# Kernel tuning notes

Measured on AMD Instinct MI355X. Metric: run time of the kernel, lower is better.

The kernel has to match this reference:

```python
import jax, jax.numpy as jnp
import numpy as np

B, WIN, D, H, O, P = 512, 128, 256, 512, 64, 64  # batch, window, input_size, hidden, output, plength


def setup_inputs() -> dict:
    key = jax.random.key(0)
    ks = jax.random.split(key, 14)
    s = 0.05
    return {
        "x": jax.random.normal(ks[0], (B, WIN, D), jnp.float32),
        # AdditiveScore params: V (v_d,), W (v_d, 2H), U (v_d, k_d) with v_d = k_d = D
        "V": jax.random.normal(ks[1], (D,), jnp.float32) * s,
        "W": jax.random.normal(ks[2], (D, 2 * H), jnp.float32) * s,
        "U": jax.random.normal(ks[3], (D, D), jnp.float32) * s,
        # LSTM (1 layer, gate order i,f,g,o): input dim D+O
        "W_ih": jax.random.normal(ks[4], (4 * H, D + O), jnp.float32) * s,
        "W_hh": jax.random.normal(ks[5], (4 * H, H), jnp.float32) * s,
        "b_ih": jax.random.normal(ks[6], (4 * H,), jnp.float32) * s,
        "b_hh": jax.random.normal(ks[7], (4 * H,), jnp.float32) * s,
        # dense: hidden -> output
        "Wd": jax.random.normal(ks[8], (O, H), jnp.float32) * s,
        "bd": jax.random.normal(ks[9], (O,), jnp.float32) * s,
        # context_s / context_c: input -> hidden
        "Ws": jax.random.normal(ks[10], (H, D), jnp.float32) * s,
        "bs": jax.random.normal(ks[11], (H,), jnp.float32) * s,
        "Wc": jax.random.normal(ks[12], (H, D), jnp.float32) * s,
        "bc": jax.random.normal(ks[13], (H,), jnp.float32) * s,
    }


def reference(x, V, W, U, W_ih, W_hh, b_ih, b_hh, Wd, bd, Ws, bs, Wc, bc):
    # initial decoder state from last encoder step
    h0 = jnp.tanh(x[:, -1] @ Ws.T + bs)            # (B, H)
    c0 = jax.nn.sigmoid(x[:, -1] @ Wc.T + bc)      # (B, H)
    y0 = jnp.zeros((x.shape[0], bd.shape[0]), x.dtype)
    # U*k is constant across decode steps: precompute once
    Uk = jnp.einsum('vd,bwd->bvw', U, x)

    def step(carry, _):
        h, c, y = carry
        q = jnp.concatenate([h, c], axis=-1)        # (B, 2H)
        Wq = q @ W.T                                # (B, D)
        # e = V^T tanh(Wq + Uk); softmax over window
        score = jnp.einsum('v,bvw->bw', V, jnp.tanh(Wq[:, :, None] + Uk))
        att = jax.nn.softmax(score, axis=-1)
        ctx = jnp.einsum('bw,bwd->bd', att, x)      # (B, D)
        inp = jnp.concatenate([y, ctx], axis=-1)    # (B, O+D)
        gates = inp @ W_ih.T + h @ W_hh.T + b_ih + b_hh
        i_, f_, g_, o_ = jnp.split(gates, 4, axis=-1)
        c_new = jax.nn.sigmoid(f_) * c + jax.nn.sigmoid(i_) * jnp.tanh(g_)
        h_new = jax.nn.sigmoid(o_) * jnp.tanh(c_new)
        y_new = h_new @ Wd.T + bd                   # (B, O)
        return (h_new, c_new, y_new), (y_new, att)

    _, (ys, atts) = jax.lax.scan(step, (h0, c0, y0), None, length=P)
    predict_y = jnp.transpose(ys, (1, 0, 2))        # (B, P, O)
    weight = jnp.transpose(atts, (1, 0, 2))
    return predict_y, weight
```

## Files before the change

### kernel.cpp

```cpp
#include <hip/hip_runtime.h>
#include <hip/hip_bf16.h>

#define B_   512
#define WIN_ 128
#define D_   256
#define H_   512
#define O_   64
#define P_   64
#define K2H  1024
#define KG   832
#define NG   2048
#define NSLN 320

typedef __attribute__((ext_vector_type(8))) short bf16x8;
typedef __attribute__((ext_vector_type(4))) float f32x4;
using bf16 = __hip_bfloat16;

__device__ __forceinline__ float fast_tanh(float x){
    float e = __expf(2.f * x);
    return 1.f - __fdividef(2.f, e + 1.f);
}
__device__ __forceinline__ float fast_sig(float x){
    return __fdividef(1.f, 1.f + __expf(-x));
}
__device__ __forceinline__ float b_lo(unsigned int u){ return __uint_as_float(u << 16); }
__device__ __forceinline__ float b_hi(unsigned int u){ return __uint_as_float(u & 0xffff0000u); }
__device__ __forceinline__ short f2bs(float v){
    return (short)__builtin_bit_cast(unsigned short, __float2bfloat16(v));
}
__device__ __forceinline__ unsigned int pack2(float a, float b){
    unsigned short sa = __builtin_bit_cast(unsigned short, __float2bfloat16(a));
    unsigned short sb = __builtin_bit_cast(unsigned short, __float2bfloat16(b));
    return (unsigned int)sa | ((unsigned int)sb << 16);
}

__global__ void k_prep(const float* __restrict__ x, const float* __restrict__ W,
                       const float* __restrict__ U, const float* __restrict__ W_ih,
                       const float* __restrict__ W_hh, const float* __restrict__ b_ih,
                       const float* __restrict__ b_hh, const float* __restrict__ Wd,
                       const float* __restrict__ Ws, const float* __restrict__ Wc,
                       bf16* __restrict__ x_bf, bf16* __restrict__ Wcomb,
                       bf16* __restrict__ Wsl, bf16* __restrict__ U_bf,
                       bf16* __restrict__ Wsc, float* __restrict__ bsum)
{
    const long NXv = (long)B_ * WIN_ * D_ / 8;
    const long NWC = (long)NG * KG;
    const long NSL = (long)8 * NSLN * 128;
    const long NU  = (long)D_ * D_;
    const long NWS = (long)K2H * D_;
    const long NB  = NG;
    const long total = NXv + NWC + NSL + NU + NWS + NB;
    for (long i = (long)blockIdx.x * blockDim.x + threadIdx.x; i < total;
         i += (long)gridDim.x * blockDim.x) {
        long j = i;
        if (j < NXv) {
            const float4* xp = (const float4*)x + j * 2;
            float4 a = xp[0], b = xp[1];
            bf16x8 v;
            v[0] = f2bs(a.x); v[1] = f2bs(a.y); v[2] = f2bs(a.z); v[3] = f2bs(a.w);
            v[4] = f2bs(b.x); v[5] = f2bs(b.y); v[6] = f2bs(b.z); v[7] = f2bs(b.w);
            *(bf16x8*)((short*)x_bf + j * 8) = v;
            continue;
        }
        j -= NXv;
        if (j < NWC) {
            long n = j / KG, k = j % KG;
            float v = (k < 320) ? W_ih[n * 320 + k] : W_hh[n * 512 + (k - 320)];
            Wcomb[j] = __float2bfloat16(v); continue;
        }
        j -= NWC;
        if (j < NSL) {
            long by = j / (NSLN * 128);
            long rem = j % (NSLN * 128);
            long n = rem / 128, k = rem % 128;
            float v;
            if (n < 256) v = (k < 64) ? W[n * K2H + by * 64 + k]
                                      : W[n * K2H + 512 + by * 64 + (k - 64)];
            else         v = (k < 64) ? Wd[(n - 256) * H_ + by * 64 + k] : 0.f;
            Wsl[j] = __float2bfloat16(v); continue;
        }
        j -= NSL;
        if (j < NU) { U_bf[j] = __float2bfloat16(U[j]); continue; }
        j -= NU;
        if (j < NWS) {
            long n = j / D_, k = j % D_;
            float v = (n < 512) ? Ws[n * D_ + k] : Wc[(n - 512) * D_ + k];
            Wsc[j] = __float2bfloat16(v); continue;
        }
        j -= NWS;
        bsum[j] = b_ih[j] + b_hh[j];
    }
}

__global__ void __launch_bounds__(256) k_init2(const bf16* __restrict__ x_bf,
                       const bf16* __restrict__ Wsc, const float* __restrict__ bs,
                       const float* __restrict__ bc, bf16* __restrict__ q_buf,
                       bf16* __restrict__ A0, float* __restrict__ c_f32)
{
    int wave = threadIdx.x >> 6, lane = threadIdx.x & 63;
    int m0 = blockIdx.x * 16;
    int n0 = blockIdx.y * 64 + wave * 16;
    int r = lane & 15, ko = (lane >> 4) * 8, rj = (lane >> 4) * 4;
    const short* xp = (const short*)x_bf;
    const short* wp = (const short*)Wsc;
    f32x4 acc = {};
    #pragma unroll
    for (int k0 = 0; k0 < D_; k0 += 32) {
        bf16x8 a  = *(const bf16x8*)(xp + (long)(m0 + r) * (WIN_ * D_) + 127 * D_ + k0 + ko);
        bf16x8 bb = *(const bf16x8*)(wp + (long)(n0 + r) * D_ + k0 + ko);
        acc = __builtin_amdgcn_mfma_f32_16x16x32_bf16(a, bb, acc, 0, 0, 0);
    }
    int n = n0 + r;
    if (n0 < 512) {
        float bias = bs[n];
        #pragma unroll
        for (int j = 0; j < 4; ++j) {
            int b = m0 + rj + j;
            float hv = fast_tanh(acc[j] + bias);
            bf16 hb = __float2bfloat16(hv);
            q_buf[(long)b * K2H + n]   = hb;
            A0[(long)b * KG + 320 + n] = hb;
        }
    } else {
        float bias = bc[n - 512];
        #pragma unroll
        for (int j = 0; j < 4; ++j) {
            int b = m0 + rj + j;
            float cv = fast_sig(acc[j] + bias);
            q_buf[(long)b * K2H + n]        = __float2bfloat16(cv);
            c_f32[(long)b * H_ + (n - 512)] = cv;
        }
    }
}

__global__ void __launch_bounds__(256) k_uk(const bf16* __restrict__ U_bf,
                    const bf16* __restrict__ x_bf, bf16* __restrict__ Uk)
{
    __shared__ __align__(16) short xs[64][264];
    int b  = blockIdx.y;
    int v0 = (blockIdx.x >> 1) * 64;
    int w0 = (blockIdx.x & 1) * 64;
    {
        const short* xg = (const short*)x_bf + (long)b * (WIN_ * D_) + (long)w0 * D_;
        int row = threadIdx.x >> 2, cc = (threadIdx.x & 3) * 64;
        #pragma unroll
        for (int i = 0; i < 8; ++i)
            *(bf16x8*)(&xs[row][cc + i * 8]) = *(const bf16x8*)(xg + (long)row * D_ + cc + i * 8);
    }
    __syncthreads();
    int lane = threadIdx.x & 63;
    int wave = threadIdx.x >> 6;
    int r  = lane & 15;
    int ko = (lane >> 4) * 8;
    const short* Up = (const short*)U_bf + (long)(v0 + wave * 16 + r) * D_;
    f32x4 acc[4] = {};
    #pragma unroll 2
    for (int k0 = 0; k0 < D_; k0 += 32) {
        bf16x8 a = *(const bf16x8*)(Up + k0 + ko);
        #pragma unroll
        for (int f = 0; f < 4; ++f) {
            bf16x8 bb = *(const bf16x8*)(&xs[f * 16 + r][k0 + ko]);
            acc[f] = __builtin_amdgcn_mfma_f32_16x16x32_bf16(a, bb, acc[f], 0, 0, 0);
        }
    }
    bf16* up = Uk + (long)b * (D_ * WIN_);
    int vbase = v0 + wave * 16 + (lane >> 4) * 4;
    #pragma unroll
    for (int f = 0; f < 4; ++f) {
        int w = w0 + f * 16 + r;
        #pragma unroll
        for (int j = 0; j < 4; ++j)
            up[(long)(vbase + j) * WIN_ + w] = __float2bfloat16(acc[f][j]);
    }
}

__global__ void __launch_bounds__(256) k_slab0(const bf16* __restrict__ q_buf,
                     const bf16* __restrict__ Wsl, float* __restrict__ slab)
{
    int bx = blockIdx.x, by = blockIdx.y;
    int wave = threadIdx.x >> 6, lane = threadIdx.x & 63;
    int r = lane & 15, ko = (lane >> 4) * 8, rj = (lane >> 4) * 4;
    int m0 = bx * 16;
    const short* qp = (const short*)q_buf;
    const short* wp = (const short*)Wsl + (long)by * NSLN * 128;
    #pragma unroll
    for (int i = 0; i < 5; ++i) {
        int n0 = (wave * 5 + i) * 16;
        f32x4 acc = {};
        #pragma unroll
        for (int k0 = 0; k0 < 128; k0 += 32) {
            long koff = (k0 < 64) ? (by * 64 + k0) : (512 + by * 64 + (k0 - 64));
            bf16x8 a  = *(const bf16x8*)(qp + (long)(m0 + r) * K2H + koff + ko);
            bf16x8 bb = *(const bf16x8*)(wp + (long)(n0 + r) * 128 + k0 + ko);
            acc = __builtin_amdgcn_mfma_f32_16x16x32_bf16(a, bb, acc, 0, 0, 0);
        }
        int n = n0 + r;
        #pragma unroll
        for (int j = 0; j < 4; ++j)
            slab[((long)by * B_ + m0 + rj + j) * NSLN + n] = acc[j];
    }
}

__global__ void __launch_bounds__(256) k_att(
    const bf16* __restrict__ x_bf, const bf16* __restrict__ Uk,
    const float* __restrict__ slab, const float* __restrict__ V,
    const float* __restrict__ bd, bf16* __restrict__ A_cur,
    float* __restrict__ out_y, float* __restrict__ out_w, int s)
{
    __shared__ float v_s[D_];
    __shared__ float wq_s[D_];
    __shared__ float part[4][WIN_];
    __shared__ float att_s[WIN_];
    __shared__ float cpart[2][D_];
    __shared__ float redw[4];

    const int b = blockIdx.x;
    const int t = threadIdx.x;

    v_s[t] = V[t];
    {
        float wsum = 0.f;
        #pragma unroll
        for (int by = 0; by < 8; ++by)
            wsum += slab[((long)by * B_ + b) * NSLN + t];
        wq_s[t] = wsum;
    }
    if (t < O_) {
        float yv = bd[t];
        #pragma unroll
        for (int by = 0; by < 8; ++by)
            yv += slab[((long)by * B_ + b) * NSLN + 256 + t];
        if (s > 0) {
            out_y[((long)b * P_ + (s - 1)) * O_ + t] = yv;
            A_cur[(long)b * KG + t] = __float2bfloat16(yv);
        } else {
            A_cur[(long)b * KG + t] = __float2bfloat16(0.f);
        }
    }
    __syncthreads();

    {
        int w2 = t & 63, vq = t >> 6;
        const unsigned int* ukp =
            (const unsigned int*)(Uk + (long)b * (D_ * WIN_) + (long)vq * 64 * WIN_) + w2;
        float sc0 = 0.f, sc1 = 0.f;
        #pragma unroll 8
        for (int i = 0; i < 64; ++i) {
            unsigned int u = ukp[(long)i * 64];
            int v = vq * 64 + i;
            float wqv = wq_s[v], vv = v_s[v];
            sc0 += vv * fast_tanh(wqv + b_lo(u));
            sc1 += vv * fast_tanh(wqv + b_hi(u));
        }
        part[vq][w2 * 2]     = sc0;
        part[vq][w2 * 2 + 1] = sc1;
    }
    __syncthreads();
    float e = 0.f, scw = 0.f;
    if (t < WIN_) {
        scw = part[0][t] + part[1][t] + part[2][t] + part[3][t];
        float m = scw;
        #pragma unroll
        for (int off = 32; off > 0; off >>= 1) m = fmaxf(m, __shfl_xor(m, off));
        if ((t & 63) == 0) redw[t >> 6] = m;
    }
    __syncthreads();
    if (t < WIN_) {
        float m = fmaxf(redw[0], redw[1]);
        e = __expf(scw - m);
        float l = e;
        #pragma unroll
        for (int off = 32; off > 0; off >>= 1) l += __shfl_xor(l, off);
        if ((t & 63) == 0) redw[2 + (t >> 6)] = l;
    }
    __syncthreads();
    if (t < WIN_) {
        float a = __fdividef(e, redw[2] + redw[3]);
        att_s[t] = a;
        out_w[((long)b * P_ + s) * WIN_ + t] = a;
    }
    __syncthreads();
    {
        int d2 = t & 127, wh = t >> 7;
        const unsigned int* xp =
            (const unsigned int*)(x_bf + (long)b * (WIN_ * D_) + (long)wh * 64 * D_) + d2;
        float c0 = 0.f, c1 = 0.f;
        #pragma unroll 8
        for (int i = 0; i < 64; ++i) {
            unsigned int u = xp[(long)i * 128];
            float a = att_s[wh * 64 + i];
            c0 += a * b_lo(u);
            c1 += a * b_hi(u);
        }
        cpart[wh][d2 * 2]     = c0;
        cpart[wh][d2 * 2 + 1] = c1;
    }
    __syncthreads();
    if (t < 128) {
        int d = t * 2;
        float f0 = cpart[0][d] + cpart[1][d];
        float f1 = cpart[0][d + 1] + cpart[1][d + 1];
        *(unsigned int*)(A_cur + (long)b * KG + O_ + d) = pack2(f0, f1);
    }
}

__global__ void __launch_bounds__(256) k_gates(const bf16* __restrict__ A_in,
                     const bf16* __restrict__ Wcomb, const bf16* __restrict__ Wsl,
                     const float* __restrict__ bsum, float* __restrict__ c_f32,
                     bf16* __restrict__ A_out, float* __restrict__ slab)
{
    __shared__ short lhc[16][136];
    int bx = blockIdx.x, by = blockIdx.y;
    int wave = threadIdx.x >> 6, lane = threadIdx.x & 63;
    int r = lane & 15, ko = (lane >> 4) * 8, rj = (lane >> 4) * 4;
    int m0 = bx * 16;
    int jw = by * 64 + wave * 16;
    const short* ap = (const short*)A_in;
    const short* wp = (const short*)Wcomb;
    f32x4 acc[4] = {};
    long arow = (long)(m0 + r) * KG;
    #pragma unroll 2
    for (int k0 = 0; k0 < KG; k0 += 32) {
        bf16x8 a = *(const bf16x8*)(ap + arow + k0 + ko);
        #pragma unroll
        for (int g = 0; g < 4; ++g) {
            bf16x8 bb = *(const bf16x8*)(wp + (long)(g * H_ + jw + r) * KG + k0 + ko);
            acc[g] = __builtin_amdgcn_mfma_f32_16x16x32_bf16(a, bb, acc[g], 0, 0, 0);
        }
    }
    int jj = jw + r;
    float bi = bsum[jj], bf_ = bsum[H_ + jj], bg = bsum[2*H_ + jj], bo = bsum[3*H_ + jj];
    #pragma unroll
    for (int j = 0; j < 4; ++j) {
        int b = m0 + rj + j;
        float iv = acc[0][j] + bi;
        float fv = acc[1][j] + bf_;
        float gv = acc[2][j] + bg;
        float ov = acc[3][j] + bo;
        float c_old = c_f32[(long)b * H_ + jj];
        float cn = fast_sig(fv) * c_old + fast_sig(iv) * fast_tanh(gv);
        float hn = fast_sig(ov) * fast_tanh(cn);
        c_f32[(long)b * H_ + jj] = cn;
        short hb = f2bs(hn);
        A_out[(long)b * KG + 320 + jj] = __builtin_bit_cast(bf16, (unsigned short)hb);
        lhc[rj + j][wave * 16 + r]      = hb;
        lhc[rj + j][64 + wave * 16 + r] = f2bs(cn);
    }
    __syncthreads();
    const short* wsl = (const short*)Wsl + (long)by * NSLN * 128;
    #pragma unroll
    for (int i = 0; i < 5; ++i) {
        int n0 = (wave * 5 + i) * 16;
        f32x4 pac = {};
        #pragma unroll
        for (int k0 = 0; k0 < 128; k0 += 32) {
            bf16x8 a  = *(const bf16x8*)(&lhc[r][k0 + ko]);
            bf16x8 bb = *(const bf16x8*)(wsl + (long)(n0 + r) * 128 + k0 + ko);
            pac = __builtin_amdgcn_mfma_f32_16x16x32_bf16(a, bb, pac, 0, 0, 0);
        }
        int n = n0 + r;
        #pragma unroll
        for (int j = 0; j < 4; ++j)
            slab[((long)by * B_ + m0 + rj + j) * NSLN + n] = pac[j];
    }
}

__global__ void __launch_bounds__(256) k_yfin(const float* __restrict__ slab,
                     const float* __restrict__ bd, float* __restrict__ out_y)
{
    int b = blockIdx.x * 4 + (threadIdx.x >> 6);
    int o = threadIdx.x & 63;
    float yv = bd[o];
    #pragma unroll
    for (int by = 0; by < 8; ++by)
        yv += slab[((long)by * B_ + b) * NSLN + 256 + o];
    out_y[((long)b * P_ + 63) * O_ + o] = yv;
}

extern "C" void kernel_launch(void* const* d_in, const int* in_sizes, int n_in,
                              void* d_out, int out_size, void* d_ws, size_t ws_size,
                              hipStream_t stream)
{
    const float* x    = (const float*)d_in[0];
    const float* V    = (const float*)d_in[1];
    const float* W    = (const float*)d_in[2];
    const float* U    = (const float*)d_in[3];
    const float* W_ih = (const float*)d_in[4];
    const float* W_hh = (const float*)d_in[5];
    const float* b_ih = (const float*)d_in[6];
    const float* b_hh = (const float*)d_in[7];
    const float* Wd   = (const float*)d_in[8];
    const float* bd   = (const float*)d_in[9];
    const float* Ws   = (const float*)d_in[10];
    const float* bs   = (const float*)d_in[11];
    const float* Wc   = (const float*)d_in[12];
    const float* bc   = (const float*)d_in[13];

    float* out_y = (float*)d_out;
    float* out_w = (float*)d_out + (long)B_ * P_ * O_;

    char* p = (char*)d_ws;
    auto alloc = [&](size_t bytes) { char* r = p; p += (bytes + 255) & ~(size_t)255; return r; };
    bf16*  x_bf  = (bf16*) alloc((size_t)B_ * WIN_ * D_ * 2);
    bf16*  Uk    = (bf16*) alloc((size_t)B_ * D_ * WIN_ * 2);
    bf16*  q_buf = (bf16*) alloc((size_t)B_ * K2H * 2);
    bf16*  A0    = (bf16*) alloc((size_t)B_ * KG * 2);
    bf16*  A1    = (bf16*) alloc((size_t)B_ * KG * 2);
    float* c_f32 = (float*)alloc((size_t)B_ * H_ * 4);
    float* slab  = (float*)alloc((size_t)8 * B_ * NSLN * 4);
    bf16*  Wcomb = (bf16*) alloc((size_t)NG * KG * 2);
    bf16*  Wsl   = (bf16*) alloc((size_t)8 * NSLN * 128 * 2);
    bf16*  U_bf  = (bf16*) alloc((size_t)D_ * D_ * 2);
    bf16*  Wsc   = (bf16*) alloc((size_t)K2H * D_ * 2);
    float* bsum  = (float*)alloc((size_t)NG * 4);
    bf16*  Abuf[2] = { A0, A1 };

    k_prep<<<4096, 256, 0, stream>>>(x, W, U, W_ih, W_hh, b_ih, b_hh, Wd, Ws, Wc,
                                     x_bf, Wcomb, Wsl, U_bf, Wsc, bsum);
    k_init2<<<dim3(32, 16), 256, 0, stream>>>(x_bf, Wsc, bs, bc, q_buf, A0, c_f32);
    k_uk<<<dim3(8, 512), 256, 0, stream>>>(U_bf, x_bf, Uk);
    k_slab0<<<dim3(32, 8), 256, 0, stream>>>(q_buf, Wsl, slab);

    for (int s = 0; s < P_; ++s) {
        k_att<<<512, 256, 0, stream>>>(x_bf, Uk, slab, V, bd,
                                       Abuf[s & 1], out_y, out_w, s);
        k_gates<<<dim3(32, 8), 256, 0, stream>>>(Abuf[s & 1], Wcomb, Wsl, bsum,
                                                 c_f32, Abuf[(s + 1) & 1], slab);
    }
    k_yfin<<<128, 256, 0, stream>>>(slab, bd, out_y);
}
```

Measured before the change: 2.509 ms.

## Fuse decode loop into one persistent kernel with software grid barriers

Replaces the 128 per-step launches of the attention and gates kernels with one persistent 256-block kernel that loops over all 64 decode steps. Steps are separated by an atomic-counter grid barrier, and the counter is reset in the prep kernel. Each 512-thread block now handles two batch rows of attention, using wider uint4 loads and finer partial reductions, and its first four waves then run the gates GEMM tile. This removes launch overhead and inter-kernel gaps, but adds spin-barrier cost, depends on all 256 blocks being resident at once, and leaves half the waves idle during the gates phase.

```diff
diff --git a/kernel.cpp b/kernel.cpp
--- a/kernel.cpp
+++ b/kernel.cpp
@@ -11,6 +11,7 @@
 #define KG   832
 #define NG   2048
 #define NSLN 320
+#define NBLK 256
 
 typedef __attribute__((ext_vector_type(8))) short bf16x8;
 typedef __attribute__((ext_vector_type(4))) float f32x4;
@@ -32,6 +33,22 @@
     unsigned short sa = __builtin_bit_cast(unsigned short, __float2bfloat16(a));
     unsigned short sb = __builtin_bit_cast(unsigned short, __float2bfloat16(b));
     return (unsigned int)sa | ((unsigned int)sb << 16);
+}
+
+__device__ __forceinline__ void grid_bar(unsigned int* cnt, unsigned int target)
+{
+    __syncthreads();
+    if (threadIdx.x == 0) {
+        __threadfence();
+        __hip_atomic_fetch_add(cnt, 1u, __ATOMIC_RELAXED, __HIP_MEMORY_SCOPE_AGENT);
+        int guard = 0;
+        while (__hip_atomic_load(cnt, __ATOMIC_RELAXED, __HIP_MEMORY_SCOPE_AGENT) < target) {
+            __builtin_amdgcn_s_sleep(1);
+            if (++guard > (1 << 24)) break;
+        }
+        __threadfence();
+    }
+    __syncthreads();
 }
 
 __global__ void k_prep(const float* __restrict__ x, const float* __restrict__ W,
@@ -41,8 +58,10 @@
                        const float* __restrict__ Ws, const float* __restrict__ Wc,
                        bf16* __restrict__ x_bf, bf16* __restrict__ Wcomb,
                        bf16* __restrict__ Wsl, bf16* __restrict__ U_bf,
-                       bf16* __restrict__ Wsc, float* __restrict__ bsum)
-{
+                       bf16* __restrict__ Wsc, float* __restrict__ bsum,
+                       unsigned int* __restrict__ bar_cnt)
+{
+    if (blockIdx.x == 0 && threadIdx.x == 0) *bar_cnt = 0u;
     const long NXv = (long)B_ * WIN_ * D_ / 8;
     const long NWC = (long)NG * KG;
     const long NSL = (long)8 * NSLN * 128;
@@ -201,180 +220,222 @@
     }
 }
 
-__global__ void __launch_bounds__(256) k_att(
+__global__ void __launch_bounds__(512) k_decode(
     const bf16* __restrict__ x_bf, const bf16* __restrict__ Uk,
-    const float* __restrict__ slab, const float* __restrict__ V,
-    const float* __restrict__ bd, bf16* __restrict__ A_cur,
-    float* __restrict__ out_y, float* __restrict__ out_w, int s)
+    float* __restrict__ slab, const float* __restrict__ V,
+    const float* __restrict__ bd, bf16* __restrict__ A0,
+    bf16* __restrict__ A1, float* __restrict__ out_y,
+    float* __restrict__ out_w, const bf16* __restrict__ Wcomb,
+    const bf16* __restrict__ Wsl, const float* __restrict__ bsum,
+    float* __restrict__ c_f32, unsigned int* __restrict__ bar_cnt)
 {
     __shared__ float v_s[D_];
-    __shared__ float wq_s[D_];
-    __shared__ float part[4][WIN_];
-    __shared__ float att_s[WIN_];
-    __shared__ float cpart[2][D_];
-    __shared__ float redw[4];
-
-    const int b = blockIdx.x;
-    const int t = threadIdx.x;
-
-    v_s[t] = V[t];
-    {
-        float wsum = 0.f;
+    __shared__ float wq_s[2][D_];
+    __shared__ float part[2][16][136];
+    __shared__ float att_s[2][WIN_];
+    __shared__ float cpart[2][8][264];
+    __shared__ float redw[2][4];
+    __shared__ short lhc[16][136];
+
+    const int tid  = threadIdx.x;
+    const int g    = blockIdx.x;
+    const int lane = tid & 63;
+    const int tb   = tid >> 8;
+    const int t2   = tid & 255;
+    const int b    = g * 2 + tb;
+
+    const int w16 = t2 & 15, vg = t2 >> 4;
+    const int dg  = t2 & 31, wg = t2 >> 5;
+    const int gx = g & 31, gy = g >> 5;
+    const int wave = tid >> 6;
+    const int r = lane & 15, ko = (lane >> 4) * 8, rj = (lane >> 4) * 4;
+
+    if (tid < D_) v_s[tid] = V[tid];
+
+    unsigned int bar = 0;
+
+    for (int s = 0; s < P_; ++s) {
+        bf16* A_cur = (s & 1) ? A1 : A0;
+        bf16* A_out = (s & 1) ? A0 : A1;
+
+        {
+            float wsum = 0.f;
+            #pragma unroll
+            for (int by = 0; by < 8; ++by)
+                wsum += slab[((long)by * B_ + b) * NSLN + t2];
+            wq_s[tb][t2] = wsum;
+            if (t2 < O_) {
+                if (s > 0) {
+                    float yv = bd[t2];
+                    #pragma unroll
+                    for (int by = 0; by < 8; ++by)
+                        yv += slab[((long)by * B_ + b) * NSLN + 256 + t2];
+                    out_y[((long)b * P_ + (s - 1)) * O_ + t2] = yv;
+                    A_cur[(long)b * KG + t2] = __float2bfloat16(yv);
+                } else {
+                    A_cur[(long)b * KG + t2] = __float2bfloat16(0.f);
+                }
+            }
+            __syncthreads();
+
+            {
+                const uint4* ukp = (const uint4*)((const short*)Uk + (long)b * (D_ * WIN_));
+                float scv[8] = {0.f,0.f,0.f,0.f,0.f,0.f,0.f,0.f};
+                #pragma unroll
+                for (int half = 0; half < 2; ++half) {
+                    uint4 u[8];
+                    #pragma unroll
+                    for (int i = 0; i < 8; ++i)
+                        u[i] = ukp[(long)(vg * 16 + half * 8 + i) * 16 + w16];
+                    #pragma unroll
+                    for (int i = 0; i < 8; ++i) {
+                        int v = vg * 16 + half * 8 + i;
+                        float wqv = wq_s[tb][v], vv = v_s[v];
+                        scv[0] += vv * fast_tanh(wqv + b_lo(u[i].x));
+                        scv[1] += vv * fast_tanh(wqv + b_hi(u[i].x));
+                        scv[2] += vv * fast_tanh(wqv + b_lo(u[i].y));
+                        scv[3] += vv * fast_tanh(wqv + b_hi(u[i].y));
+                        scv[4] += vv * fast_tanh(wqv + b_lo(u[i].z));
+                        scv[5] += vv * fast_tanh(wqv + b_hi(u[i].z));
+                        scv[6] += vv * fast_tanh(wqv + b_lo(u[i].w));
+                        scv[7] += vv * fast_tanh(wqv + b_hi(u[i].w));
+                    }
+                }
+                #pragma unroll
+                for (int j = 0; j < 8; ++j) part[tb][vg][w16 * 8 + j] = scv[j];
+            }
+            __syncthreads();
+
+            float e = 0.f, scw = 0.f;
+            if (t2 < WIN_) {
+                #pragma unroll
+                for (int q = 0; q < 16; ++q) scw += part[tb][q][t2];
+                float m = scw;
+                #pragma unroll
+                for (int off = 32; off > 0; off >>= 1) m = fmaxf(m, __shfl_xor(m, off));
+                if (lane == 0) redw[tb][t2 >> 6] = m;
+            }
+            __syncthreads();
+            if (t2 < WIN_) {
+                float m = fmaxf(redw[tb][0], redw[tb][1]);
+                e = __expf(scw - m);
+                float l = e;
+                #pragma unroll
+                for (int off = 32; off > 0; off >>= 1) l += __shfl_xor(l, off);
+                if (lane == 0) redw[tb][2 + (t2 >> 6)] = l;
+            }
+            __syncthreads();
+            if (t2 < WIN_) {
+                float a = __fdividef(e, redw[tb][2] + redw[tb][3]);
+                att_s[tb][t2] = a;
+                out_w[((long)b * P_ + s) * WIN_ + t2] = a;
+            }
+            __syncthreads();
+
+            {
+                const uint4* xp = (const uint4*)((const short*)x_bf + (long)b * (WIN_ * D_));
+                float cacc[8] = {0.f,0.f,0.f,0.f,0.f,0.f,0.f,0.f};
+                #pragma unroll
+                for (int half = 0; half < 2; ++half) {
+                    uint4 u[8];
+                    #pragma unroll
+                    for (int i = 0; i < 8; ++i)
+                        u[i] = xp[(long)(wg * 16 + half * 8 + i) * 32 + dg];
+                    #pragma unroll
+                    for (int i = 0; i < 8; ++i) {
+                        float a = att_s[tb][wg * 16 + half * 8 + i];
+                        cacc[0] += a * b_lo(u[i].x);
+                        cacc[1] += a * b_hi(u[i].x);
+                        cacc[2] += a * b_lo(u[i].y);
+                        cacc[3] += a * b_hi(u[i].y);
+                        cacc[4] += a * b_lo(u[i].z);
+                        cacc[5] += a * b_hi(u[i].z);
+                        cacc[6] += a * b_lo(u[i].w);
+                        cacc[7] += a * b_hi(u[i].w);
+                    }
+                }
+                #pragma unroll
+                for (int j = 0; j < 8; ++j) cpart[tb][wg][dg * 8 + j] = cacc[j];
+            }
+            __syncthreads();
+            if (t2 < 128) {
+                int d = t2 * 2;
+                float f0 = 0.f, f1 = 0.f;
+                #pragma unroll
+                for (int q = 0; q < 8; ++q) { f0 += cpart[tb][q][d]; f1 += cpart[tb][q][d + 1]; }
+                *(unsigned int*)(A_cur + (long)b * KG + O_ + d) = pack2(f0, f1);
+            }
+        }
+        ++bar; grid_bar(bar_cnt, NBLK * bar);
+
+        if (wave < 4) {
+            int m0 = gx * 16;
+            int jw = gy * 64 + wave * 16;
+            const short* ap = (const short*)A_cur;
+            const short* wp = (const short*)Wcomb;
+            f32x4 acc[4] = {};
+            long arow = (long)(m0 + r) * KG;
+            #pragma unroll 2
+            for (int k0 = 0; k0 < KG; k0 += 32) {
+                bf16x8 a = *(const bf16x8*)(ap + arow + k0 + ko);
+                #pragma unroll
+                for (int gq = 0; gq < 4; ++gq) {
+                    bf16x8 bb = *(const bf16x8*)(wp + (long)(gq * H_ + jw + r) * KG + k0 + ko);
+                    acc[gq] = __builtin_amdgcn_mfma_f32_16x16x32_bf16(a, bb, acc[gq], 0, 0, 0);
+                }
+            }
+            int jj = jw + r;
+            float bi = bsum[jj], bf_ = bsum[H_ + jj];
+            float bg2 = bsum[2 * H_ + jj], bo = bsum[3 * H_ + jj];
+            #pragma unroll
+            for (int j = 0; j < 4; ++j) {
+                int bb2 = m0 + rj + j;
+                float iv = acc[0][j] + bi;
+                float fv = acc[1][j] + bf_;
+                float gv = acc[2][j] + bg2;
+                float ov = acc[3][j] + bo;
+                float c_old = c_f32[(long)bb2 * H_ + jj];
+                float cn = fast_sig(fv) * c_old + fast_sig(iv) * fast_tanh(gv);
+                float hn = fast_sig(ov) * fast_tanh(cn);
+                c_f32[(long)bb2 * H_ + jj] = cn;
+                short hb = f2bs(hn);
+                A_out[(long)bb2 * KG + 320 + jj] = __builtin_bit_cast(bf16, (unsigned short)hb);
+                lhc[rj + j][wave * 16 + r]      = hb;
+                lhc[rj + j][64 + wave * 16 + r] = f2bs(cn);
+            }
+        }
+        __syncthreads();
+        if (wave < 4) {
+            int m0 = gx * 16;
+            const short* wsl = (const short*)Wsl + (long)gy * NSLN * 128;
+            #pragma unroll
+            for (int i = 0; i < 5; ++i) {
+                int n0 = (wave * 5 + i) * 16;
+                f32x4 pac = {};
+                #pragma unroll
+                for (int k0 = 0; k0 < 128; k0 += 32) {
+                    bf16x8 a  = *(const bf16x8*)(&lhc[r][k0 + ko]);
+                    bf16x8 bb = *(const bf16x8*)(wsl + (long)(n0 + r) * 128 + k0 + ko);
+                    pac = __builtin_amdgcn_mfma_f32_16x16x32_bf16(a, bb, pac, 0, 0, 0);
+                }
+                int n = n0 + r;
+                #pragma unroll
+                for (int j = 0; j < 4; ++j)
+                    slab[((long)gy * B_ + m0 + rj + j) * NSLN + n] = pac[j];
+            }
+        }
+        ++bar; grid_bar(bar_cnt, NBLK * bar);
+    }
+
+    if (tid < 128) {
+        int bb2 = g * 2 + (tid >> 6);
+        int o = tid & 63;
+        float yv = bd[o];
         #pragma unroll
         for (int by = 0; by < 8; ++by)
-            wsum += slab[((long)by * B_ + b) * NSLN + t];
-        wq_s[t] = wsum;
-    }
-    if (t < O_) {
-        float yv = bd[t];
-        #pragma unroll
-        for (int by = 0; by < 8; ++by)
-            yv += slab[((long)by * B_ + b) * NSLN + 256 + t];
-        if (s > 0) {
-            out_y[((long)b * P_ + (s - 1)) * O_ + t] = yv;
-            A_cur[(long)b * KG + t] = __float2bfloat16(yv);
-        } else {
-            A_cur[(long)b * KG + t] = __float2bfloat16(0.f);
-        }
-    }
-    __syncthreads();
-
-    {
-        int w2 = t & 63, vq = t >> 6;
-        const unsigned int* ukp =
-            (const unsigned int*)(Uk + (long)b * (D_ * WIN_) + (long)vq * 64 * WIN_) + w2;
-        float sc0 = 0.f, sc1 = 0.f;
-        #pragma unroll 8
-        for (int i = 0; i < 64; ++i) {
-            unsigned int u = ukp[(long)i * 64];
-            int v = vq * 64 + i;
-            float wqv = wq_s[v], vv = v_s[v];
-            sc0 += vv * fast_tanh(wqv + b_lo(u));
-            sc1 += vv * fast_tanh(wqv + b_hi(u));
-        }
-        part[vq][w2 * 2]     = sc0;
-        part[vq][w2 * 2 + 1] = sc1;
-    }
-    __syncthreads();
-    float e = 0.f, scw = 0.f;
-    if (t < WIN_) {
-        scw = part[0][t] + part[1][t] + part[2][t] + part[3][t];
-        float m = scw;
-        #pragma unroll
-        for (int off = 32; off > 0; off >>= 1) m = fmaxf(m, __shfl_xor(m, off));
-        if ((t & 63) == 0) redw[t >> 6] = m;
-    }
-    __syncthreads();
-    if (t < WIN_) {
-        float m = fmaxf(redw[0], redw[1]);
-        e = __expf(scw - m);
-        float l = e;
-        #pragma unroll
-        for (int off = 32; off > 0; off >>= 1) l += __shfl_xor(l, off);
-        if ((t & 63) == 0) redw[2 + (t >> 6)] = l;
-    }
-    __syncthreads();
-    if (t < WIN_) {
-        float a = __fdividef(e, redw[2] + redw[3]);
-        att_s[t] = a;
-        out_w[((long)b * P_ + s) * WIN_ + t] = a;
-    }
-    __syncthreads();
-    {
-        int d2 = t & 127, wh = t >> 7;
-        const unsigned int* xp =
-            (const unsigned int*)(x_bf + (long)b * (WIN_ * D_) + (long)wh * 64 * D_) + d2;
-        float c0 = 0.f, c1 = 0.f;
-        #pragma unroll 8
-        for (int i = 0; i < 64; ++i) {
-            unsigned int u = xp[(long)i * 128];
-            float a = att_s[wh * 64 + i];
-            c0 += a * b_lo(u);
-            c1 += a * b_hi(u);
-        }
-        cpart[wh][d2 * 2]     = c0;
-        cpart[wh][d2 * 2 + 1] = c1;
-    }
-    __syncthreads();
-    if (t < 128) {
-        int d = t * 2;
-        float f0 = cpart[0][d] + cpart[1][d];
-        float f1 = cpart[0][d + 1] + cpart[1][d + 1];
-        *(unsigned int*)(A_cur + (long)b * KG + O_ + d) = pack2(f0, f1);
-    }
-}
-
-__global__ void __launch_bounds__(256) k_gates(const bf16* __restrict__ A_in,
-                     const bf16* __restrict__ Wcomb, const bf16* __restrict__ Wsl,
-                     const float* __restrict__ bsum, float* __restrict__ c_f32,
-                     bf16* __restrict__ A_out, float* __restrict__ slab)
-{
-    __shared__ short lhc[16][136];
-    int bx = blockIdx.x, by = blockIdx.y;
-    int wave = threadIdx.x >> 6, lane = threadIdx.x & 63;
-    int r = lane & 15, ko = (lane >> 4) * 8, rj = (lane >> 4) * 4;
-    int m0 = bx * 16;
-    int jw = by * 64 + wave * 16;
-    const short* ap = (const short*)A_in;
-    const short* wp = (const short*)Wcomb;
-    f32x4 acc[4] = {};
-    long arow = (long)(m0 + r) * KG;
-    #pragma unroll 2
-    for (int k0 = 0; k0 < KG; k0 += 32) {
-        bf16x8 a = *(const bf16x8*)(ap + arow + k0 + ko);
-        #pragma unroll
-        for (int g = 0; g < 4; ++g) {
-            bf16x8 bb = *(const bf16x8*)(wp + (long)(g * H_ + jw + r) * KG + k0 + ko);
-            acc[g] = __builtin_amdgcn_mfma_f32_16x16x32_bf16(a, bb, acc[g], 0, 0, 0);
-        }
-    }
-    int jj = jw + r;
-    float bi = bsum[jj], bf_ = bsum[H_ + jj], bg = bsum[2*H_ + jj], bo = bsum[3*H_ + jj];
-    #pragma unroll
-    for (int j = 0; j < 4; ++j) {
-        int b = m0 + rj + j;
-        float iv = acc[0][j] + bi;
-        float fv = acc[1][j] + bf_;
-        float gv = acc[2][j] + bg;
-        float ov = acc[3][j] + bo;
-        float c_old = c_f32[(long)b * H_ + jj];
-        float cn = fast_sig(fv) * c_old + fast_sig(iv) * fast_tanh(gv);
-        float hn = fast_sig(ov) * fast_tanh(cn);
-        c_f32[(long)b * H_ + jj] = cn;
-        short hb = f2bs(hn);
-        A_out[(long)b * KG + 320 + jj] = __builtin_bit_cast(bf16, (unsigned short)hb);
-        lhc[rj + j][wave * 16 + r]      = hb;
-        lhc[rj + j][64 + wave * 16 + r] = f2bs(cn);
-    }
-    __syncthreads();
-    const short* wsl = (const short*)Wsl + (long)by * NSLN * 128;
-    #pragma unroll
-    for (int i = 0; i < 5; ++i) {
-        int n0 = (wave * 5 + i) * 16;
-        f32x4 pac = {};
-        #pragma unroll
-        for (int k0 = 0; k0 < 128; k0 += 32) {
-            bf16x8 a  = *(const bf16x8*)(&lhc[r][k0 + ko]);
-            bf16x8 bb = *(const bf16x8*)(wsl + (long)(n0 + r) * 128 + k0 + ko);
-            pac = __builtin_amdgcn_mfma_f32_16x16x32_bf16(a, bb, pac, 0, 0, 0);
-        }
-        int n = n0 + r;
-        #pragma unroll
-        for (int j = 0; j < 4; ++j)
-            slab[((long)by * B_ + m0 + rj + j) * NSLN + n] = pac[j];
-    }
-}
-
-__global__ void __launch_bounds__(256) k_yfin(const float* __restrict__ slab,
-                     const float* __restrict__ bd, float* __restrict__ out_y)
-{
-    int b = blockIdx.x * 4 + (threadIdx.x >> 6);
-    int o = threadIdx.x & 63;
-    float yv = bd[o];
-    #pragma unroll
-    for (int by = 0; by < 8; ++by)
-        yv += slab[((long)by * B_ + b) * NSLN + 256 + o];
-    out_y[((long)b * P_ + 63) * O_ + o] = yv;
+            yv += slab[((long)by * B_ + bb2) * NSLN + 256 + o];
+        out_y[((long)bb2 * P_ + 63) * O_ + o] = yv;
+    }
 }
 
 extern "C" void kernel_launch(void* const* d_in, const int* in_sizes, int n_in,
@@ -413,19 +474,15 @@
     bf16*  U_bf  = (bf16*) alloc((size_t)D_ * D_ * 2);
     bf16*  Wsc   = (bf16*) alloc((size_t)K2H * D_ * 2);
     float* bsum  = (float*)alloc((size_t)NG * 4);
-    bf16*  Abuf[2] = { A0, A1 };
+    unsigned int* bar_cnt = (unsigned int*)alloc(256);
 
     k_prep<<<4096, 256, 0, stream>>>(x, W, U, W_ih, W_hh, b_ih, b_hh, Wd, Ws, Wc,
-                                     x_bf, Wcomb, Wsl, U_bf, Wsc, bsum);
+                                     x_bf, Wcomb, Wsl, U_bf, Wsc, bsum, bar_cnt);
     k_init2<<<dim3(32, 16), 256, 0, stream>>>(x_bf, Wsc, bs, bc, q_buf, A0, c_f32);
     k_uk<<<dim3(8, 512), 256, 0, stream>>>(U_bf, x_bf, Uk);
     k_slab0<<<dim3(32, 8), 256, 0, stream>>>(q_buf, Wsl, slab);
 
-    for (int s = 0; s < P_; ++s) {
-        k_att<<<512, 256, 0, stream>>>(x_bf, Uk, slab, V, bd,
-                                       Abuf[s & 1], out_y, out_w, s);
-        k_gates<<<dim3(32, 8), 256, 0, stream>>>(Abuf[s & 1], Wcomb, Wsl, bsum,
-                                                 c_f32, Abuf[(s + 1) & 1], slab);
-    }
-    k_yfin<<<128, 256, 0, stream>>>(slab, bd, out_y);
-}
+    k_decode<<<NBLK, 512, 0, stream>>>(x_bf, Uk, slab, V, bd, A0, A1,
+                                       out_y, out_w, Wcomb, Wsl, bsum,
+                                       c_f32, bar_cnt);
+}
```

After: 7.755 ms. 3.09x slower.

## Vectorize attention score and context loops with 16-byte loads and finer partitioning

Applied to the files above, without the earlier changes.

Rewrites the score and context loops in the per-step attention kernel so each thread issues 128-bit loads covering 8 bf16 values, batching 8 loads before compute. The old code used 32-bit strided loads. Work is split into 16 v-groups and 8 w-groups, with padded shared-memory partial buffers and a longer final reduction. The k_uk shared-memory staging pattern is changed to coalesce global loads, and the prep kernel grid is doubled. The aim is better memory-level parallelism and fewer load instructions, at the cost of more registers and reduction work.

```diff
diff --git a/kernel.cpp b/kernel.cpp
--- a/kernel.cpp
+++ b/kernel.cpp
@@ -142,10 +142,10 @@
     int w0 = (blockIdx.x & 1) * 64;
     {
         const short* xg = (const short*)x_bf + (long)b * (WIN_ * D_) + (long)w0 * D_;
-        int row = threadIdx.x >> 2, cc = (threadIdx.x & 3) * 64;
+        int row = threadIdx.x >> 2, c4 = (threadIdx.x & 3) * 8;
         #pragma unroll
         for (int i = 0; i < 8; ++i)
-            *(bf16x8*)(&xs[row][cc + i * 8]) = *(const bf16x8*)(xg + (long)row * D_ + cc + i * 8);
+            *(bf16x8*)(&xs[row][c4 + i * 32]) = *(const bf16x8*)(xg + (long)row * D_ + c4 + i * 32);
     }
     __syncthreads();
     int lane = threadIdx.x & 63;
@@ -209,13 +209,14 @@
 {
     __shared__ float v_s[D_];
     __shared__ float wq_s[D_];
-    __shared__ float part[4][WIN_];
+    __shared__ float part[16][136];
     __shared__ float att_s[WIN_];
-    __shared__ float cpart[2][D_];
+    __shared__ float cpart[8][264];
     __shared__ float redw[4];
 
     const int b = blockIdx.x;
     const int t = threadIdx.x;
+    const int lane = t & 63;
 
     v_s[t] = V[t];
     {
@@ -226,11 +227,11 @@
         wq_s[t] = wsum;
     }
     if (t < O_) {
-        float yv = bd[t];
-        #pragma unroll
-        for (int by = 0; by < 8; ++by)
-            yv += slab[((long)by * B_ + b) * NSLN + 256 + t];
         if (s > 0) {
+            float yv = bd[t];
+            #pragma unroll
+            for (int by = 0; by < 8; ++by)
+                yv += slab[((long)by * B_ + b) * NSLN + 256 + t];
             out_y[((long)b * P_ + (s - 1)) * O_ + t] = yv;
             A_cur[(long)b * KG + t] = __float2bfloat16(yv);
         } else {
@@ -240,29 +241,42 @@
     __syncthreads();
 
     {
-        int w2 = t & 63, vq = t >> 6;
-        const unsigned int* ukp =
-            (const unsigned int*)(Uk + (long)b * (D_ * WIN_) + (long)vq * 64 * WIN_) + w2;
-        float sc0 = 0.f, sc1 = 0.f;
-        #pragma unroll 8
-        for (int i = 0; i < 64; ++i) {
-            unsigned int u = ukp[(long)i * 64];
-            int v = vq * 64 + i;
-            float wqv = wq_s[v], vv = v_s[v];
-            sc0 += vv * fast_tanh(wqv + b_lo(u));
-            sc1 += vv * fast_tanh(wqv + b_hi(u));
-        }
-        part[vq][w2 * 2]     = sc0;
-        part[vq][w2 * 2 + 1] = sc1;
-    }
-    __syncthreads();
+        const int w16 = t & 15, vg = t >> 4;
+        const uint4* ukp = (const uint4*)((const short*)Uk + (long)b * (D_ * WIN_));
+        float scv[8] = {0.f,0.f,0.f,0.f,0.f,0.f,0.f,0.f};
+        #pragma unroll
+        for (int half = 0; half < 2; ++half) {
+            uint4 u[8];
+            #pragma unroll
+            for (int i = 0; i < 8; ++i)
+                u[i] = ukp[(long)(vg * 16 + half * 8 + i) * 16 + w16];
+            #pragma unroll
+            for (int i = 0; i < 8; ++i) {
+                int v = vg * 16 + half * 8 + i;
+                float wqv = wq_s[v], vv = v_s[v];
+                scv[0] += vv * fast_tanh(wqv + b_lo(u[i].x));
+                scv[1] += vv * fast_tanh(wqv + b_hi(u[i].x));
+                scv[2] += vv * fast_tanh(wqv + b_lo(u[i].y));
+                scv[3] += vv * fast_tanh(wqv + b_hi(u[i].y));
+                scv[4] += vv * fast_tanh(wqv + b_lo(u[i].z));
+                scv[5] += vv * fast_tanh(wqv + b_hi(u[i].z));
+                scv[6] += vv * fast_tanh(wqv + b_lo(u[i].w));
+                scv[7] += vv * fast_tanh(wqv + b_hi(u[i].w));
+            }
+        }
+        #pragma unroll
+        for (int j = 0; j < 8; ++j) part[vg][w16 * 8 + j] = scv[j];
+    }
+    __syncthreads();
+
     float e = 0.f, scw = 0.f;
     if (t < WIN_) {
-        scw = part[0][t] + part[1][t] + part[2][t] + part[3][t];
+        #pragma unroll
+        for (int q = 0; q < 16; ++q) scw += part[q][t];
         float m = scw;
         #pragma unroll
         for (int off = 32; off > 0; off >>= 1) m = fmaxf(m, __shfl_xor(m, off));
-        if ((t & 63) == 0) redw[t >> 6] = m;
+        if (lane == 0) redw[t >> 6] = m;
     }
     __syncthreads();
     if (t < WIN_) {
@@ -271,7 +285,7 @@
         float l = e;
         #pragma unroll
         for (int off = 32; off > 0; off >>= 1) l += __shfl_xor(l, off);
-        if ((t & 63) == 0) redw[2 + (t >> 6)] = l;
+        if (lane == 0) redw[2 + (t >> 6)] = l;
     }
     __syncthreads();
     if (t < WIN_) {
@@ -280,26 +294,39 @@
         out_w[((long)b * P_ + s) * WIN_ + t] = a;
     }
     __syncthreads();
+
     {
-        int d2 = t & 127, wh = t >> 7;
-        const unsigned int* xp =
-            (const unsigned int*)(x_bf + (long)b * (WIN_ * D_) + (long)wh * 64 * D_) + d2;
-        float c0 = 0.f, c1 = 0.f;
-        #pragma unroll 8
-        for (int i = 0; i < 64; ++i) {
-            unsigned int u = xp[(long)i * 128];
-            float a = att_s[wh * 64 + i];
-            c0 += a * b_lo(u);
-            c1 += a * b_hi(u);
-        }
-        cpart[wh][d2 * 2]     = c0;
-        cpart[wh][d2 * 2 + 1] = c1;
+        const int dg = t & 31, wg = t >> 5;
+        const uint4* xp = (const uint4*)((const short*)x_bf + (long)b * (WIN_ * D_));
+        float cacc[8] = {0.f,0.f,0.f,0.f,0.f,0.f,0.f,0.f};
+        #pragma unroll
+        for (int half = 0; half < 2; ++half) {
+            uint4 u[8];
+            #pragma unroll
+            for (int i = 0; i < 8; ++i)
+                u[i] = xp[(long)(wg * 16 + half * 8 + i) * 32 + dg];
+            #pragma unroll
+            for (int i = 0; i < 8; ++i) {
+                float a = att_s[wg * 16 + half * 8 + i];
+                cacc[0] += a * b_lo(u[i].x);
+                cacc[1] += a * b_hi(u[i].x);
+                cacc[2] += a * b_lo(u[i].y);
+                cacc[3] += a * b_hi(u[i].y);
+                cacc[4] += a * b_lo(u[i].z);
+                cacc[5] += a * b_hi(u[i].z);
+                cacc[6] += a * b_lo(u[i].w);
+                cacc[7] += a * b_hi(u[i].w);
+            }
+        }
+        #pragma unroll
+        for (int j = 0; j < 8; ++j) cpart[wg][dg * 8 + j] = cacc[j];
     }
     __syncthreads();
     if (t < 128) {
         int d = t * 2;
-        float f0 = cpart[0][d] + cpart[1][d];
-        float f1 = cpart[0][d + 1] + cpart[1][d + 1];
+        float f0 = 0.f, f1 = 0.f;
+        #pragma unroll
+        for (int q = 0; q < 8; ++q) { f0 += cpart[q][d]; f1 += cpart[q][d + 1]; }
         *(unsigned int*)(A_cur + (long)b * KG + O_ + d) = pack2(f0, f1);
     }
 }
@@ -415,7 +442,7 @@
     float* bsum  = (float*)alloc((size_t)NG * 4);
     bf16*  Abuf[2] = { A0, A1 };
 
-    k_prep<<<4096, 256, 0, stream>>>(x, W, U, W_ih, W_hh, b_ih, b_hh, Wd, Ws, Wc,
+    k_prep<<<8192, 256, 0, stream>>>(x, W, U, W_ih, W_hh, b_ih, b_hh, Wd, Ws, Wc,
                                      x_bf, Wcomb, Wsl, U_bf, Wsc, bsum);
     k_init2<<<dim3(32, 16), 256, 0, stream>>>(x_bf, Wsc, bs, bc, q_buf, A0, c_f32);
     k_uk<<<dim3(8, 512), 256, 0, stream>>>(U_bf, x_bf, Uk);
```

Measured after the change: 2.577 ms. 2.7% more time.
